# Performance work log

Hardware: AMD Instinct MI355X
Metric: run time of the kernel (lower is better)

The kernel has to match this reference:

```python
import jax, jax.numpy as jnp
import numpy as np
import math

G, B, L, C = 4, 4, 512, 768
NH, DH = 12, 64  # num heads, head dim; NH*DH == C

def setup_inputs() -> dict:
    key = jax.random.key(0)
    ks = jax.random.split(key, 8)
    s = 0.02
    return {
        "hidden_states": jax.random.normal(ks[0], (G, B, L, C), jnp.float32),
        "attention_mask": jnp.zeros((G, B, 1, 1, L), jnp.float32),
        "query_weight": jax.random.normal(ks[1], (G, C, C), jnp.float32) * s,
        "query_bias": jax.random.normal(ks[2], (G, 1, C), jnp.float32) * s,
        "key_weight": jax.random.normal(ks[3], (G, C, C), jnp.float32) * s,
        "key_bias": jax.random.normal(ks[4], (G, 1, C), jnp.float32) * s,
        "value_weight": jax.random.normal(ks[5], (G, C, C), jnp.float32) * s,
        "value_bias": jax.random.normal(ks[6], (G, 1, C), jnp.float32) * s,
    }

def _heads(x):
    # [g, b*l, c] -> [g, b, nh, l, dh]
    return x.reshape(G, B, L, NH, DH).transpose(0, 1, 3, 2, 4)

def reference(hidden_states, attention_mask, query_weight, query_bias,
              key_weight, key_bias, value_weight, value_bias):
    hs = hidden_states.reshape(G, B * L, C)
    q = _heads(jnp.einsum('gtc,gcd->gtd', hs, query_weight) + query_bias)
    k = _heads(jnp.einsum('gtc,gcd->gtd', hs, key_weight) + key_bias)
    v = _heads(jnp.einsum('gtc,gcd->gtd', hs, value_weight) + value_bias)
    scale = 1.0 / math.sqrt(DH)
    scores = jnp.einsum('gbhld,gbhmd->gbhlm', q, k) * scale + attention_mask
    probs = jax.nn.softmax(scores, axis=-1)  # dropout prob = 0.0 -> identity
    ctx = jnp.einsum('gbhlm,gbhmd->gbhld', probs, v)
    ctx = ctx.transpose(0, 1, 3, 2, 4).reshape(G, B, L, NH * DH)
    return ctx
```

## Files before the change

kernel.cpp:

```cpp
#include <hip/hip_runtime.h>

#define G_ 4
#define B_ 4
#define L_ 512
#define C_ 768
#define NH_ 12
#define DH_ 64
#define T_ 2048

typedef __bf16 bf16x8 __attribute__((ext_vector_type(8)));
typedef float f32x4 __attribute__((ext_vector_type(4)));
typedef unsigned int u32x4 __attribute__((ext_vector_type(4)));
typedef unsigned short u16;
typedef unsigned short u16x4 __attribute__((ext_vector_type(4)));

__device__ __forceinline__ u16 f2bf(float x) {
    unsigned u = __builtin_bit_cast(unsigned, x);
    u = (u + 0x7FFFu + ((u >> 16) & 1u)) >> 16;
    return (u16)u;
}

__device__ __forceinline__ void gload16(const void* g, unsigned lds_off) {
    __builtin_amdgcn_global_load_lds(
        (const __attribute__((address_space(1))) unsigned int*)(uintptr_t)g,
        (__attribute__((address_space(3))) unsigned int*)(uintptr_t)(size_t)lds_off,
        16, 0, 0);
}

__global__ void k_convert(const float* __restrict__ in, u16* __restrict__ out, int n4) {
    int i = blockIdx.x * blockDim.x + threadIdx.x;
    if (i >= n4) return;
    float4 v = reinterpret_cast<const float4*>(in)[i];
    u16x4 o;
    o.x = f2bf(v.x); o.y = f2bf(v.y); o.z = f2bf(v.z); o.w = f2bf(v.w);
    reinterpret_cast<u16x4*>(out)[i] = o;
}

__global__ void k_transpose(const float* __restrict__ wq, const float* __restrict__ wk,
                            const float* __restrict__ wv, u16* __restrict__ wt) {
    __shared__ u16 tile[32][33];
    int qkv = blockIdx.z >> 2, g = blockIdx.z & 3;
    const float* W = (qkv == 0 ? wq : qkv == 1 ? wk : wv) + g * (C_ * C_);
    u16* O = wt + blockIdx.z * (C_ * C_);
    int d0 = blockIdx.x * 32, c0 = blockIdx.y * 32;
    int tx = threadIdx.x, ty = threadIdx.y;
#pragma unroll
    for (int j = 0; j < 4; j++)
        tile[ty + 8 * j][tx] = f2bf(W[(c0 + ty + 8 * j) * C_ + d0 + tx]);
    __syncthreads();
#pragma unroll
    for (int j = 0; j < 4; j++)
        O[(d0 + ty + 8 * j) * C_ + c0 + tx] = tile[tx][ty + 8 * j];
}

#define BM 128
#define BN 128
#define BK 64

__global__ __launch_bounds__(256) void k_qkv_gemm(
    const u16* __restrict__ hsb, const u16* __restrict__ wt,
    const float* __restrict__ qb, const float* __restrict__ kb,
    const float* __restrict__ vb, u16* __restrict__ qkvout, u16* __restrict__ vtout) {
    __shared__ u16 Asm[BM * BK];
    __shared__ u16 Bsm[BN * BK];
    int qkv = blockIdx.z >> 2, g = blockIdx.z & 3;
    int n0 = blockIdx.x * BN, m0 = blockIdx.y * BM;
    const u16* Ag = hsb + g * (T_ * C_);
    const u16* Bg = wt + blockIdx.z * (C_ * C_);
    const float* bias = (qkv == 0 ? qb : qkv == 1 ? kb : vb) + g * C_;
    u16* Og = qkvout + qkv * (G_ * T_ * C_) + g * (T_ * C_);

    int tid = threadIdx.x, lane = tid & 63, w = tid >> 6;
    int wm = (w >> 1) * 64, wn = (w & 1) * 64;
    int l15 = lane & 15, l4 = lane >> 4;
    unsigned abase = (unsigned)(uintptr_t)Asm;
    unsigned bbase = (unsigned)(uintptr_t)Bsm;

    f32x4 acc[4][4];
#pragma unroll
    for (int a = 0; a < 4; a++)
#pragma unroll
        for (int b = 0; b < 4; b++) acc[a][b] = (f32x4){0.f, 0.f, 0.f, 0.f};

    for (int k0 = 0; k0 < C_; k0 += BK) {
#pragma unroll
        for (int it = 0; it < 4; it++) {
            int s = it * 256 + tid;
            int v = s ^ ((s >> 3) & 7);
            int r = v >> 3, c8 = v & 7;
            unsigned lb = (unsigned)((it * 256 + w * 64) * 16);
            gload16(Ag + (m0 + r) * C_ + k0 + c8 * 8, abase + lb);
            gload16(Bg + (n0 + r) * C_ + k0 + c8 * 8, bbase + lb);
        }
        __syncthreads();
        const char* Ac = (const char*)Asm;
        const char* Bc = (const char*)Bsm;
#pragma unroll
        for (int kk = 0; kk < 2; kk++) {
            bf16x8 af[4], bfr[4];
#pragma unroll
            for (int mi = 0; mi < 4; mi++) {
                int row = wm + mi * 16 + l15;
                unsigned off = (unsigned)(row * 128 + kk * 64 + l4 * 16) ^ (unsigned)((row & 7) << 4);
                af[mi] = __builtin_bit_cast(bf16x8, *reinterpret_cast<const u32x4*>(Ac + off));
            }
#pragma unroll
            for (int ni = 0; ni < 4; ni++) {
                int row = wn + ni * 16 + l15;
                unsigned off = (unsigned)(row * 128 + kk * 64 + l4 * 16) ^ (unsigned)((row & 7) << 4);
                bfr[ni] = __builtin_bit_cast(bf16x8, *reinterpret_cast<const u32x4*>(Bc + off));
            }
#pragma unroll
            for (int mi = 0; mi < 4; mi++)
#pragma unroll
                for (int ni = 0; ni < 4; ni++)
                    acc[mi][ni] = __builtin_amdgcn_mfma_f32_16x16x32_bf16(
                        af[mi], bfr[ni], acc[mi][ni], 0, 0, 0);
        }
        __syncthreads();
    }
    if (qkv == 2) {
#pragma unroll
        for (int ni = 0; ni < 4; ni++) {
            int col = n0 + wn + ni * 16 + l15;
            int h = col >> 6, d = col & 63;
            float bv = bias[col];
#pragma unroll
            for (int mi = 0; mi < 4; mi++) {
#pragma unroll
                for (int i = 0; i < 4; i++) {
                    int row = m0 + wm + mi * 16 + l4 * 4 + i;
                    int bb = row >> 9, l = row & 511;
                    vtout[(((g * B_ + bb) * NH_ + h) * DH_ + d) * L_ + l] =
                        f2bf(acc[mi][ni][i] + bv);
                }
            }
        }
    } else {
#pragma unroll
        for (int ni = 0; ni < 4; ni++) {
            int col = n0 + wn + ni * 16 + l15;
            float bv = bias[col];
#pragma unroll
            for (int mi = 0; mi < 4; mi++) {
#pragma unroll
                for (int i = 0; i < 4; i++) {
                    int row = m0 + wm + mi * 16 + l4 * 4 + i;
                    Og[row * C_ + col] = f2bf(acc[mi][ni][i] + bv);
                }
            }
        }
    }
}

#define SCALE 0.125f
#define LDP 72

__global__ __launch_bounds__(256) void k_attn(
    const u16* __restrict__ qkv, const u16* __restrict__ vt,
    const float* __restrict__ mask, float* __restrict__ out) {
    __shared__ u16 Ksm[64 * 64];
    __shared__ u16 Vsm[64 * 64];
    __shared__ u16 Psm[64 * LDP];
    __shared__ float msk[L_];

    int bid = blockIdx.x;
    int head = bid % (G_ * B_ * NH_);
    int qt = bid / (G_ * B_ * NH_);
    int h = head % NH_, gb = head / NH_;
    int g = gb >> 2, b = gb & 3;
    int q0 = qt * 64;
    int tid = threadIdx.x, lane = tid & 63, w = tid >> 6;
    int l15 = lane & 15, l4 = lane >> 4;

    const int QKVSZ = G_ * T_ * C_;
    const u16* Qg = qkv + g * (T_ * C_) + (b * L_) * C_ + h * DH_;
    const u16* Kg = Qg + QKVSZ;
    const u16* VtH = vt + (size_t)(gb * NH_ + h) * (DH_ * L_);

    unsigned kbase = (unsigned)(uintptr_t)Ksm;
    unsigned vbase = (unsigned)(uintptr_t)Vsm;

    for (int i = tid; i < L_; i += 256) msk[i] = mask[gb * L_ + i];

    bf16x8 qf[2];
#pragma unroll
    for (int kk = 0; kk < 2; kk++)
        qf[kk] = __builtin_bit_cast(bf16x8, *reinterpret_cast<const u32x4*>(
                     Qg + (q0 + w * 16 + l15) * C_ + kk * 32 + l4 * 8));

    float mrun[4], lrun[4];
    f32x4 accO[4];
#pragma unroll
    for (int i = 0; i < 4; i++) { mrun[i] = -1e30f; lrun[i] = 0.f; }
#pragma unroll
    for (int df = 0; df < 4; df++) accO[df] = (f32x4){0.f, 0.f, 0.f, 0.f};

    for (int kt = 0; kt < 8; kt++) {
        int krow0 = kt * 64;

#pragma unroll
        for (int it = 0; it < 2; it++) {
            int s = it * 256 + tid;
            int v = s ^ ((s >> 3) & 7);
            int r = v >> 3, c8 = v & 7;
            unsigned lb = (unsigned)((it * 256 + w * 64) * 16);
            gload16(Kg + (krow0 + r) * C_ + c8 * 8, kbase + lb);
            gload16(VtH + r * L_ + krow0 + c8 * 8, vbase + lb);
        }
        __syncthreads();

        const char* Kc = (const char*)Ksm;
        const char* Vc = (const char*)Vsm;
        f32x4 s4[4];
#pragma unroll
        for (int nf = 0; nf < 4; nf++) s4[nf] = (f32x4){0.f, 0.f, 0.f, 0.f};
#pragma unroll
        for (int kk = 0; kk < 2; kk++) {
#pragma unroll
            for (int nf = 0; nf < 4; nf++) {
                int row = nf * 16 + l15;
                unsigned off = (unsigned)(row * 128 + kk * 64 + l4 * 16) ^ (unsigned)((row & 7) << 4);
                bf16x8 kf = __builtin_bit_cast(bf16x8, *reinterpret_cast<const u32x4*>(Kc + off));
                s4[nf] = __builtin_amdgcn_mfma_f32_16x16x32_bf16(qf[kk], kf, s4[nf], 0, 0, 0);
            }
        }

        float mv[4];
#pragma unroll
        for (int nf = 0; nf < 4; nf++) mv[nf] = msk[krow0 + nf * 16 + l15];

        float p[4][4];
#pragma unroll
        for (int i = 0; i < 4; i++) {
            float sv[4];
#pragma unroll
            for (int nf = 0; nf < 4; nf++) sv[nf] = fmaf(s4[nf][i], SCALE, mv[nf]);
            float mx = fmaxf(fmaxf(sv[0], sv[1]), fmaxf(sv[2], sv[3]));
            mx = fmaxf(mx, __shfl_xor(mx, 1));
            mx = fmaxf(mx, __shfl_xor(mx, 2));
            mx = fmaxf(mx, __shfl_xor(mx, 4));
            mx = fmaxf(mx, __shfl_xor(mx, 8));
            float mn = fmaxf(mrun[i], mx);
            float alpha = __expf(mrun[i] - mn);
            mrun[i] = mn;
            float rs = 0.f;
#pragma unroll
            for (int nf = 0; nf < 4; nf++) { p[nf][i] = __expf(sv[nf] - mn); rs += p[nf][i]; }
            rs += __shfl_xor(rs, 1);
            rs += __shfl_xor(rs, 2);
            rs += __shfl_xor(rs, 4);
            rs += __shfl_xor(rs, 8);
            lrun[i] = lrun[i] * alpha + rs;
#pragma unroll
            for (int df = 0; df < 4; df++) accO[df][i] *= alpha;
        }

#pragma unroll
        for (int nf = 0; nf < 4; nf++)
#pragma unroll
            for (int i = 0; i < 4; i++)
                Psm[(w * 16 + l4 * 4 + i) * LDP + nf * 16 + l15] = f2bf(p[nf][i]);

#pragma unroll
        for (int kk = 0; kk < 2; kk++) {
            bf16x8 pf = __builtin_bit_cast(bf16x8, *reinterpret_cast<const u32x4*>(
                            &Psm[(w * 16 + l15) * LDP + kk * 32 + l4 * 8]));
#pragma unroll
            for (int df = 0; df < 4; df++) {
                int row = df * 16 + l15;
                unsigned off = (unsigned)(row * 128 + kk * 64 + l4 * 16) ^ (unsigned)((row & 7) << 4);
                bf16x8 vf = __builtin_bit_cast(bf16x8, *reinterpret_cast<const u32x4*>(Vc + off));
                accO[df] = __builtin_amdgcn_mfma_f32_16x16x32_bf16(pf, vf, accO[df], 0, 0, 0);
            }
        }
        __syncthreads();
    }

#pragma unroll
    for (int i = 0; i < 4; i++) {
        float inv = 1.0f / lrun[i];
        int row = q0 + w * 16 + l4 * 4 + i;
#pragma unroll
        for (int df = 0; df < 4; df++)
            out[((g * B_ + b) * L_ + row) * C_ + h * DH_ + df * 16 + l15] =
                accO[df][i] * inv;
    }
}

extern "C" void kernel_launch(void* const* d_in, const int* in_sizes, int n_in,
                              void* d_out, int out_size, void* d_ws, size_t ws_size,
                              hipStream_t stream) {
    (void)in_sizes; (void)n_in; (void)out_size; (void)ws_size;
    const float* hs = (const float*)d_in[0];
    const float* mask = (const float*)d_in[1];
    const float* qw = (const float*)d_in[2];
    const float* qb = (const float*)d_in[3];
    const float* kw = (const float*)d_in[4];
    const float* kb = (const float*)d_in[5];
    const float* vw = (const float*)d_in[6];
    const float* vb = (const float*)d_in[7];
    float* out = (float*)d_out;

    char* ws = (char*)d_ws;
    const size_t OFF_WT = (size_t)G_ * T_ * C_ * 2;
    const size_t OFF_QKV = OFF_WT + (size_t)3 * G_ * C_ * C_ * 2;
    u16* hsb = (u16*)ws;
    u16* wt = (u16*)(ws + OFF_WT);
    u16* qkvb = (u16*)(ws + OFF_QKV);
    u16* vtb = qkvb + 2 * (size_t)G_ * T_ * C_;

    int n4 = (G_ * T_ * C_) / 4;
    k_convert<<<(n4 + 255) / 256, 256, 0, stream>>>(hs, hsb, n4);
    k_transpose<<<dim3(C_ / 32, C_ / 32, 12), dim3(32, 8), 0, stream>>>(qw, kw, vw, wt);
    k_qkv_gemm<<<dim3(C_ / BN, T_ / BM, 12), 256, 0, stream>>>(hsb, wt, qb, kb, vb, qkvb, vtb);
    k_attn<<<dim3(L_ / 64 * NH_ * G_ * B_), 256, 0, stream>>>(qkvb, vtb, mask, out);
}
```

Before: 211.0 us.

## Double-buffer LDS tiles in QKV GEMM and attention, remap GEMM blocks per XCD

Both the QKV projection GEMM and the attention kernel now keep two LDS buffers and prefetch the next K-tile (or K/V tile) while the current one is consumed by MFMAs. This removes the trailing barrier per iteration and hides global-to-LDS load latency behind compute. The GEMM also moves to a 1D grid whose block index is permuted so consecutive blocks on the same XCD share A/B tiles, aiming at better L2 reuse. The cost is doubled LDS per block, which may lower occupancy.

```diff
diff --git a/kernel.cpp b/kernel.cpp
--- a/kernel.cpp
+++ b/kernel.cpp
@@ -56,25 +56,32 @@
 #define BM 128
 #define BN 128
 #define BK 64
+#define NKS 12
 
 __global__ __launch_bounds__(256) void k_qkv_gemm(
     const u16* __restrict__ hsb, const u16* __restrict__ wt,
     const float* __restrict__ qb, const float* __restrict__ kb,
     const float* __restrict__ vb, u16* __restrict__ qkvout, u16* __restrict__ vtout) {
-    __shared__ u16 Asm[BM * BK];
-    __shared__ u16 Bsm[BN * BK];
-    int qkv = blockIdx.z >> 2, g = blockIdx.z & 3;
-    int n0 = blockIdx.x * BN, m0 = blockIdx.y * BM;
+    __shared__ u16 Asm[2][BM * BK];
+    __shared__ u16 Bsm[2][BN * BK];
+
+    int bid = blockIdx.x;
+    int lin = (bid & 7) * 144 + (bid >> 3);
+    int zz = lin / 96, r96 = lin % 96;
+    int y = r96 / 6, x = r96 % 6;
+    int g = zz / 3, qkv = zz % 3;
+    int n0 = x * BN, m0 = y * BM;
+
     const u16* Ag = hsb + g * (T_ * C_);
-    const u16* Bg = wt + blockIdx.z * (C_ * C_);
+    const u16* Bg = wt + (qkv * 4 + g) * (C_ * C_);
     const float* bias = (qkv == 0 ? qb : qkv == 1 ? kb : vb) + g * C_;
     u16* Og = qkvout + qkv * (G_ * T_ * C_) + g * (T_ * C_);
 
     int tid = threadIdx.x, lane = tid & 63, w = tid >> 6;
     int wm = (w >> 1) * 64, wn = (w & 1) * 64;
     int l15 = lane & 15, l4 = lane >> 4;
-    unsigned abase = (unsigned)(uintptr_t)Asm;
-    unsigned bbase = (unsigned)(uintptr_t)Bsm;
+    unsigned abase = (unsigned)(uintptr_t)&Asm[0][0];
+    unsigned bbase = (unsigned)(uintptr_t)&Bsm[0][0];
 
     f32x4 acc[4][4];
 #pragma unroll
@@ -82,19 +89,27 @@
 #pragma unroll
         for (int b = 0; b < 4; b++) acc[a][b] = (f32x4){0.f, 0.f, 0.f, 0.f};
 
-    for (int k0 = 0; k0 < C_; k0 += BK) {
+    auto stage = [&](int k0, int buf) {
+        unsigned ab = abase + (unsigned)(buf * 16384);
+        unsigned bb = bbase + (unsigned)(buf * 16384);
 #pragma unroll
         for (int it = 0; it < 4; it++) {
             int s = it * 256 + tid;
             int v = s ^ ((s >> 3) & 7);
-            int r = v >> 3, c8 = v & 7;
+            int rr = v >> 3, c8 = v & 7;
             unsigned lb = (unsigned)((it * 256 + w * 64) * 16);
-            gload16(Ag + (m0 + r) * C_ + k0 + c8 * 8, abase + lb);
-            gload16(Bg + (n0 + r) * C_ + k0 + c8 * 8, bbase + lb);
-        }
+            gload16(Ag + (m0 + rr) * C_ + k0 + c8 * 8, ab + lb);
+            gload16(Bg + (n0 + rr) * C_ + k0 + c8 * 8, bb + lb);
+        }
+    };
+
+    stage(0, 0);
+    int cur = 0;
+    for (int ks = 0; ks < NKS; ks++) {
         __syncthreads();
-        const char* Ac = (const char*)Asm;
-        const char* Bc = (const char*)Bsm;
+        if (ks < NKS - 1) stage((ks + 1) * BK, cur ^ 1);
+        const char* Ac = (const char*)&Asm[0][0] + cur * 16384;
+        const char* Bc = (const char*)&Bsm[0][0] + cur * 16384;
 #pragma unroll
         for (int kk = 0; kk < 2; kk++) {
             bf16x8 af[4], bfr[4];
@@ -117,7 +132,7 @@
                     acc[mi][ni] = __builtin_amdgcn_mfma_f32_16x16x32_bf16(
                         af[mi], bfr[ni], acc[mi][ni], 0, 0, 0);
         }
-        __syncthreads();
+        cur ^= 1;
     }
     if (qkv == 2) {
 #pragma unroll
@@ -159,8 +174,8 @@
 __global__ __launch_bounds__(256) void k_attn(
     const u16* __restrict__ qkv, const u16* __restrict__ vt,
     const float* __restrict__ mask, float* __restrict__ out) {
-    __shared__ u16 Ksm[64 * 64];
-    __shared__ u16 Vsm[64 * 64];
+    __shared__ u16 Ksm[2][64 * 64];
+    __shared__ u16 Vsm[2][64 * 64];
     __shared__ u16 Psm[64 * LDP];
     __shared__ float msk[L_];
 
@@ -178,8 +193,8 @@
     const u16* Kg = Qg + QKVSZ;
     const u16* VtH = vt + (size_t)(gb * NH_ + h) * (DH_ * L_);
 
-    unsigned kbase = (unsigned)(uintptr_t)Ksm;
-    unsigned vbase = (unsigned)(uintptr_t)Vsm;
+    unsigned kbase = (unsigned)(uintptr_t)&Ksm[0][0];
+    unsigned vbase = (unsigned)(uintptr_t)&Vsm[0][0];
 
     for (int i = tid; i < L_; i += 256) msk[i] = mask[gb * L_ + i];
 
@@ -196,22 +211,30 @@
 #pragma unroll
     for (int df = 0; df < 4; df++) accO[df] = (f32x4){0.f, 0.f, 0.f, 0.f};
 
-    for (int kt = 0; kt < 8; kt++) {
+    auto stage = [&](int kt, int buf) {
         int krow0 = kt * 64;
-
+        unsigned kb = kbase + (unsigned)(buf * 8192);
+        unsigned vbb = vbase + (unsigned)(buf * 8192);
 #pragma unroll
         for (int it = 0; it < 2; it++) {
             int s = it * 256 + tid;
             int v = s ^ ((s >> 3) & 7);
-            int r = v >> 3, c8 = v & 7;
+            int rr = v >> 3, c8 = v & 7;
             unsigned lb = (unsigned)((it * 256 + w * 64) * 16);
-            gload16(Kg + (krow0 + r) * C_ + c8 * 8, kbase + lb);
-            gload16(VtH + r * L_ + krow0 + c8 * 8, vbase + lb);
-        }
+            gload16(Kg + (krow0 + rr) * C_ + c8 * 8, kb + lb);
+            gload16(VtH + rr * L_ + krow0 + c8 * 8, vbb + lb);
+        }
+    };
+
+    stage(0, 0);
+    int cur = 0;
+    for (int kt = 0; kt < 8; kt++) {
+        int krow0 = kt * 64;
         __syncthreads();
-
-        const char* Kc = (const char*)Ksm;
-        const char* Vc = (const char*)Vsm;
+        if (kt < 7) stage(kt + 1, cur ^ 1);
+
+        const char* Kc = (const char*)&Ksm[0][0] + cur * 8192;
+        const char* Vc = (const char*)&Vsm[0][0] + cur * 8192;
         f32x4 s4[4];
 #pragma unroll
         for (int nf = 0; nf < 4; nf++) s4[nf] = (f32x4){0.f, 0.f, 0.f, 0.f};
@@ -274,7 +297,7 @@
                 accO[df] = __builtin_amdgcn_mfma_f32_16x16x32_bf16(pf, vf, accO[df], 0, 0, 0);
             }
         }
-        __syncthreads();
+        cur ^= 1;
     }
 
 #pragma unroll
@@ -313,6 +336,6 @@
     int n4 = (G_ * T_ * C_) / 4;
     k_convert<<<(n4 + 255) / 256, 256, 0, stream>>>(hs, hsb, n4);
     k_transpose<<<dim3(C_ / 32, C_ / 32, 12), dim3(32, 8), 0, stream>>>(qw, kw, vw, wt);
-    k_qkv_gemm<<<dim3(C_ / BN, T_ / BM, 12), 256, 0, stream>>>(hsb, wt, qb, kb, vb, qkvb, vtb);
+    k_qkv_gemm<<<dim3(1152), 256, 0, stream>>>(hsb, wt, qb, kb, vb, qkvb, vtb);
     k_attn<<<dim3(L_ / 64 * NH_ * G_ * B_), 256, 0, stream>>>(qkvb, vtb, mask, out);
 }
```

Result: faster. 205.6 us (-2.6%).
